# Performance work log

Measured on AMD Instinct MI355X. Metric: run time of the kernel, lower is better.

## Reference

```python
import jax, jax.numpy as jnp
import numpy as np

B, S, D = 8, 4096, 256
H, DK, DV = 8, 32, 32


def _layer_norm(x, g, b, eps=1e-6):
    mu = jnp.mean(x, axis=-1, keepdims=True)
    var = jnp.mean(jnp.square(x - mu), axis=-1, keepdims=True)
    return (x - mu) * jax.lax.rsqrt(var + eps) * g + b


def setup_inputs() -> dict:
    key = jax.random.key(0)
    ks = jax.random.split(key, 16)
    std = 1.0 / np.sqrt(D)
    p = lambda k, shp: (jax.random.normal(k, shp, jnp.float32) * std)
    return {
        "h": jax.random.normal(ks[0], (B, S, D), jnp.float32),
        "e": jax.random.normal(ks[1], (B, S, D), jnp.float32),
        "s": jax.random.normal(ks[2], (B, D), jnp.float32),
        "sat_wq": p(ks[3], (D, H * DK)), "sat_wk": p(ks[4], (D, H * DK)),
        "sat_wv": p(ks[5], (D, H * DV)), "sat_wo": p(ks[6], (H * DV, D)),
        "sat_g": jnp.ones((D,), jnp.float32), "sat_b": jnp.zeros((D,), jnp.float32),
        "rel_wq": p(ks[7], (D, H * DK)), "rel_wk": p(ks[8], (D, H * DK)),
        "rel_wv": p(ks[9], (D, H * DV)), "rel_wo": p(ks[10], (H * DV, D)),
        "rel_g": jnp.ones((D,), jnp.float32), "rel_b": jnp.zeros((D,), jnp.float32),
    }


def reference(h, e, s, sat_wq, sat_wk, sat_wv, sat_wo, sat_g, sat_b,
              rel_wq, rel_wk, rel_wv, rel_wo, rel_g, rel_b):
    b, sl, d = h.shape
    scale = 1.0 / np.sqrt(DK)

    # ---- build 5-token context: [left, self, right, entity, relay] ----
    hp = jnp.pad(h, ((0, 0), (1, 1), (0, 0)))  # zeros at both ends
    s_exp = jnp.broadcast_to(s[:, None, :], (b, sl, d))
    ctx = jnp.stack([hp[:, :sl], h, hp[:, 2:], e, s_exp], axis=2)  # [B,S,5,D]

    # ---- satellite attention: 1 query vs 5-token context per position ----
    q = (h @ sat_wq).reshape(b, sl, H, DK)
    k = (ctx @ sat_wk).reshape(b, sl, 5, H, DK)
    v = (ctx @ sat_wv).reshape(b, sl, 5, H, DV)
    attn = jax.nn.softmax(jnp.einsum('bshd,bschd->bshc', q, k) * scale, axis=-1)
    o = jnp.einsum('bshc,bschd->bshd', attn, v).reshape(b, sl, H * DV) @ sat_wo
    h_out = _layer_norm(o + h, sat_g, sat_b)  # [B,S,D]

    # ---- relay attention: relay query vs [s; h_out] ----
    s_h = jnp.concatenate([s[:, None, :], h_out], axis=1)  # [B,S+1,D]
    qr = (s @ rel_wq).reshape(b, H, DK)
    kr = (s_h @ rel_wk).reshape(b, sl + 1, H, DK)
    vr = (s_h @ rel_wv).reshape(b, sl + 1, H, DV)
    attn_r = jax.nn.softmax(jnp.einsum('bhd,bkhd->bhk', qr, kr) * scale, axis=-1)
    orl = jnp.einsum('bhk,bkhd->bhd', attn_r, vr).reshape(b, H * DV) @ rel_wo
    s_out = _layer_norm(orl + s, rel_g, rel_b)  # [B,D]

    return (h_out, s_out)
```

## Files before the change

### kernel.cpp

```cpp
#include <hip/hip_runtime.h>
#include <hip/hip_bf16.h>

typedef unsigned short ushort_t;
typedef unsigned int uint_t;
typedef __attribute__((ext_vector_type(8))) short bf16x8;
typedef __attribute__((ext_vector_type(4))) float f32x4;

#define NB 8
#define NS 4096
#define ND 256
#define NH 8
#define NDK 32
#define NBS (NB*NS)
#define NK  (NS+1)
#define CH  513
#define NCH 8
static const size_t PBUF = (size_t)NB*(NS+1)*ND;
static const size_t HSZ  = (size_t)NBS*ND;

__device__ __forceinline__ ushort_t f2b(float x){
  union { __hip_bfloat16 b; ushort_t u; } cv; cv.b = __float2bfloat16(x); return cv.u;
}
__device__ __forceinline__ float b2f(ushort_t u){
  union { uint_t u; float f; } cv; cv.u = ((uint_t)u) << 16; return cv.f;
}
__device__ __forceinline__ void gload16(const ushort_t* g, ushort_t* l){
  __builtin_amdgcn_global_load_lds(
      (const __attribute__((address_space(1))) void*)g,
      (__attribute__((address_space(3))) void*)l, 16, 0, 0);
}
__device__ __forceinline__ uint4 packbf16x8(float4 a, float4 b){
  uint4 p;
  p.x = f2b(a.x) | ((uint_t)f2b(a.y)<<16);
  p.y = f2b(a.z) | ((uint_t)f2b(a.w)<<16);
  p.z = f2b(b.x) | ((uint_t)f2b(b.y)<<16);
  p.w = f2b(b.z) | ((uint_t)f2b(b.w)<<16);
  return p;
}

__device__ __forceinline__ float bsum256(float v){
  __shared__ float tmp[4];
  #pragma unroll
  for (int o=32;o>0;o>>=1) v += __shfl_down(v,o);
  if ((threadIdx.x & 63)==0) tmp[threadIdx.x>>6] = v;
  __syncthreads();
  float r = tmp[0]+tmp[1]+tmp[2]+tmp[3];
  __syncthreads();
  return r;
}

__global__ __launch_bounds__(256) void prep(
    const float* __restrict__ w0, const float* __restrict__ w1, const float* __restrict__ w2,
    const float* __restrict__ w3, const float* __restrict__ w4, const float* __restrict__ w5,
    ushort_t* __restrict__ WtAll,
    const float* __restrict__ s,
    const float* __restrict__ rwq,
    ushort_t* __restrict__ ksb, ushort_t* __restrict__ vsb,
    float* __restrict__ qr, ushort_t* __restrict__ krv)
{
  __shared__ float sh[64*68];
  const int blk = blockIdx.x;
  const int tid = threadIdx.x;
  if (blk < 96){
    const int z = blk >> 4, xy = blk & 15;
    const float* W = (z==0)?w0:(z==1)?w1:(z==2)?w2:(z==3)?w3:(z==4)?w4:w5;
    ushort_t* Wt = WtAll + (size_t)z*65536;
    float (*t)[68] = (float(*)[68])sh;
    const int k0 = (xy>>2)*64, n0 = (xy&3)*64;
    const int tr = tid>>4, tc4 = (tid&15)*4;
    #pragma unroll
    for (int i=0;i<4;i++){
      int r = tr + i*16;
      float4 v = *(const float4*)&W[(size_t)(k0+r)*ND + n0 + tc4];
      t[r][tc4]=v.x; t[r][tc4+1]=v.y; t[r][tc4+2]=v.z; t[r][tc4+3]=v.w;
    }
    __syncthreads();
    #pragma unroll
    for (int i=0;i<4;i++){
      int n = tr + i*16;
      uint_t q0 = f2b(t[tc4+0][n]) | ((uint_t)f2b(t[tc4+1][n])<<16);
      uint_t q1 = f2b(t[tc4+2][n]) | ((uint_t)f2b(t[tc4+3][n])<<16);
      *(uint2*)&Wt[(size_t)(n0+n)*ND + k0 + tc4] = make_uint2(q0,q1);
    }
  } else {
    const int rem = blk - 96;
    const int b = rem & 7, which = rem >> 3;
    const float* W = (which==0)?w1:(which==1)?w2:(which==2)?rwq:(which==3)?w4:w5;
    float* a = sh;
    a[tid] = s[(size_t)b*ND + tid];
    __syncthreads();
    float acc = 0.f;
    #pragma unroll 8
    for (int d=0; d<ND; d++)
      acc = fmaf(a[d], W[(size_t)d*ND + tid], acc);
    switch (which){
      case 0: ksb[(size_t)b*ND + tid] = f2b(acc); break;
      case 1: vsb[(size_t)b*ND + tid] = f2b(acc); break;
      case 2: qr[(size_t)b*ND + tid] = acc; break;
      case 3: krv[(size_t)b*NK*512 + tid] = f2b(acc); break;
      default: krv[(size_t)b*NK*512 + 256 + tid] = f2b(acc); break;
    }
  }
}

__global__ __launch_bounds__(512) void gemm_qkve(const float* __restrict__ hA,
    const float* __restrict__ eA, const ushort_t* __restrict__ Wt,
    ushort_t* __restrict__ hQKV, ushort_t* __restrict__ eKV)
{
  __shared__ __align__(16) ushort_t Ap[64][256];
  __shared__ __align__(16) ushort_t Bs[2][128][64];
  const int blk = blockIdx.x;
  const bool isH = blk < 512;
  const float* A = isH ? hA : eA;
  const ushort_t* Wb = isH ? Wt : (Wt + 65536);
  ushort_t* Y = isH ? hQKV : eKV;
  const int ldn  = isH ? 768 : 512;
  const int ncol = isH ? 6 : 4;
  const int row0 = (blk & 511) * 64;
  const int tid = threadIdx.x;
  const int lane = tid & 63;
  const int wave = tid >> 6;
  const int wr  = (wave>>2)*32;
  const int wcw = (wave&3)*32;
  const int l15 = lane & 15, lg = lane >> 4;
  const int lr8 = lane >> 3;
  const int ls  = (lane & 7) ^ lr8;

  #pragma unroll
  for (int i=0;i<4;i++){
    int sgi = tid + i*512;
    int r   = sgi >> 5;
    int c8  = (sgi & 31) * 8;
    const float* ga = A + (size_t)(row0 + r)*ND + c8;
    float4 a0 = *(const float4*)ga, a1 = *(const float4*)(ga+4);
    int byte = r*512 + ((c8*2) ^ ((r&7)<<4));
    *(uint4*)((char*)&Ap[0][0] + byte) = packbf16x8(a0,a1);
  }

  const ushort_t* Bbase = Wb + (size_t)(wave*16 + lr8)*ND + ls*8;
  #define STAGEB(ct, kt, bb) do{ \
    const ushort_t* bp = Bbase + (size_t)(ct)*128*ND + (kt)*64; \
    gload16(bp,                &Bs[bb][wave*16][0]); \
    gload16(bp + (size_t)8*ND, &Bs[bb][wave*16+8][0]); \
  }while(0)

  const f32x4 vzero = {0.f,0.f,0.f,0.f};
  f32x4 acc[2][2] = {};
  STAGEB(0,0,0);
  __syncthreads();
  int buf = 0;
  const int total = ncol*4;
  for (int s = 0; s < total; ++s){
    const int kt = s & 3;
    if (s+1 < total) STAGEB((s+1)>>2, (s+1)&3, buf^1);
    #pragma unroll
    for (int ks=0; ks<2; ks++){
      bf16x8 af[2], bfr[2];
      #pragma unroll
      for (int mi=0;mi<2;mi++){
        int ra  = wr + mi*16 + l15;
        int cb2 = kt*128 + ks*64 + lg*16;
        af[mi] = *(const bf16x8*)((const char*)&Ap[0][0] + ra*512 + (cb2 ^ ((ra&7)<<4)));
      }
      #pragma unroll
      for (int ni=0;ni<2;ni++){
        int rb = wcw + ni*16 + l15;
        int cb = (ks<<6) + (lg<<4);
        bfr[ni] = *(const bf16x8*)((const char*)&Bs[buf][0][0] + rb*128 + (cb ^ ((rb&7)<<4)));
      }
      #pragma unroll
      for (int mi=0;mi<2;mi++)
        #pragma unroll
        for (int ni=0;ni<2;ni++)
          acc[mi][ni] = __builtin_amdgcn_mfma_f32_16x16x32_bf16(af[mi], bfr[ni], acc[mi][ni], 0,0,0);
    }
    __syncthreads();
    buf ^= 1;
    if (kt == 3){
      const int col0 = (s >> 2) * 128;
      #pragma unroll
      for (int mi=0;mi<2;mi++)
        #pragma unroll
        for (int r=0;r<4;r++){
          size_t orow = (size_t)(row0 + wr + mi*16 + lg*4 + r);
          #pragma unroll
          for (int ni=0;ni<2;ni++)
            Y[orow*(size_t)ldn + col0 + wcw + ni*16 + l15] = f2b(acc[mi][ni][r]);
        }
      #pragma unroll
      for (int mi=0;mi<2;mi++)
        #pragma unroll
        for (int ni=0;ni<2;ni++)
          acc[mi][ni] = vzero;
    }
  }
  #undef STAGEB
}

__global__ __launch_bounds__(512) void gemm_krv(const ushort_t* __restrict__ A,
    const ushort_t* __restrict__ Wt, ushort_t* __restrict__ Y)
{
  __shared__ __align__(16) ushort_t As[2][128][64];
  __shared__ __align__(16) ushort_t Bs[2][128][64];
  const int tid  = threadIdx.x;
  const int row0 = blockIdx.x*128;
  const int col0 = blockIdx.y*128;
  const int lane = tid & 63;
  const int wave = tid >> 6;
  const int wr = (wave>>2)*64;
  const int wc = (wave&3)*32;
  const int l15 = lane & 15, lg = lane >> 4;
  const int lr8 = lane >> 3;
  const int ls  = (lane & 7) ^ lr8;

  const ushort_t* Asrc = A  + (size_t)(row0 + wave*16 + lr8)*ND + ls*8;
  const ushort_t* Bsrc = Wt + (size_t)(col0 + wave*16 + lr8)*ND + ls*8;

  f32x4 acc[4][2] = {};

  #define STAGE(t, bb) do{ \
    gload16(Asrc + (t)*64,                &As[bb][wave*16][0]); \
    gload16(Asrc + (size_t)8*ND + (t)*64, &As[bb][wave*16+8][0]); \
    gload16(Bsrc + (t)*64,                &Bs[bb][wave*16][0]); \
    gload16(Bsrc + (size_t)8*ND + (t)*64, &Bs[bb][wave*16+8][0]); \
  }while(0)
  #define COMPUTE(bb) do{ \
    _Pragma("unroll") \
    for (int ks=0; ks<2; ks++){ \
      bf16x8 af[4], bfr[2]; \
      _Pragma("unroll") \
      for (int mi=0;mi<4;mi++){ \
        int ra = wr + mi*16 + l15; int cb = (ks<<6) + (lg<<4); \
        af[mi] = *(const bf16x8*)((const char*)&As[bb][0][0] + ra*128 + (cb ^ ((ra&7)<<4))); \
      } \
      _Pragma("unroll") \
      for (int ni=0;ni<2;ni++){ \
        int rb = wc + ni*16 + l15; int cb = (ks<<6) + (lg<<4); \
        bfr[ni] = *(const bf16x8*)((const char*)&Bs[bb][0][0] + rb*128 + (cb ^ ((rb&7)<<4))); \
      } \
      _Pragma("unroll") \
      for (int mi=0;mi<4;mi++) \
        _Pragma("unroll") \
        for (int ni=0;ni<2;ni++) \
          acc[mi][ni] = __builtin_amdgcn_mfma_f32_16x16x32_bf16(af[mi], bfr[ni], acc[mi][ni], 0,0,0); \
    } \
  }while(0)

  STAGE(0, 0);
  __syncthreads();
  STAGE(1, 1); COMPUTE(0); __syncthreads();
  STAGE(2, 0); COMPUTE(1); __syncthreads();
  STAGE(3, 1); COMPUTE(0); __syncthreads();
  COMPUTE(1);
  #undef STAGE
  #undef COMPUTE

  #pragma unroll
  for (int mi=0;mi<4;mi++)
    #pragma unroll
    for (int r=0;r<4;r++){
      int row = row0 + wr + mi*16 + lg*4 + r;
      size_t orow = (size_t)(row>>12)*NK + 1 + (row&4095);
      #pragma unroll
      for (int ni=0;ni<2;ni++)
        Y[orow*512 + col0 + wc + ni*16 + l15] = f2b(acc[mi][ni][r]);
    }
}

__global__ __launch_bounds__(512) void oproj_ln(const ushort_t* __restrict__ A,
    const ushort_t* __restrict__ Wt, const float* __restrict__ hres,
    const float* __restrict__ g, const float* __restrict__ bta,
    float* __restrict__ outf, ushort_t* __restrict__ outb)
{
  __shared__ __align__(16) ushort_t As[2][64][64];
  __shared__ float rs[64][4], rq[64][4];
  __shared__ float gl[ND], bl[ND];
  const int tid  = threadIdx.x;
  const int row0 = blockIdx.x*64;
  const int lane = tid & 63;
  const int wave = tid >> 6;
  const int wr = (wave>>2)*32;
  const int wc = (wave&3)*64;
  const int l15 = lane & 15, lg = lane >> 4;
  const int lr8 = lane >> 3;
  const int ls  = (lane & 7) ^ lr8;

  if (tid < ND){ gl[tid] = g[tid]; bl[tid] = bta[tid]; }

  const ushort_t* Asrc = A + (size_t)(row0 + wave*8 + lr8)*ND + ls*8;

  f32x4 acc[2][4] = {};

  #define STAGE3(t, bb) gload16(Asrc + (t)*64, &As[bb][wave*8][0])
  #define COMPUTE3(t, bb) do{ \
    _Pragma("unroll") \
    for (int ks=0; ks<2; ks++){ \
      bf16x8 af[2], bfr[4]; \
      _Pragma("unroll") \
      for (int mi=0;mi<2;mi++){ \
        int ra = wr + mi*16 + l15; int cb = (ks<<6) + (lg<<4); \
        af[mi] = *(const bf16x8*)((const char*)&As[bb][0][0] + ra*128 + (cb ^ ((ra&7)<<4))); \
      } \
      _Pragma("unroll") \
      for (int ni=0;ni<4;ni++) \
        bfr[ni] = *(const bf16x8*)&Wt[(size_t)(wc + ni*16 + l15)*ND + (t)*64 + ks*32 + lg*8]; \
      _Pragma("unroll") \
      for (int mi=0;mi<2;mi++) \
        _Pragma("unroll") \
        for (int ni=0;ni<4;ni++) \
          acc[mi][ni] = __builtin_amdgcn_mfma_f32_16x16x32_bf16(af[mi], bfr[ni], acc[mi][ni], 0,0,0); \
    } \
  }while(0)

  STAGE3(0, 0);
  __syncthreads();
  STAGE3(1, 1); COMPUTE3(0, 0); __syncthreads();
  STAGE3(2, 0); COMPUTE3(1, 1); __syncthreads();
  STAGE3(3, 1); COMPUTE3(2, 0); __syncthreads();
  COMPUTE3(3, 1);
  #undef STAGE3
  #undef COMPUTE3

  #pragma unroll
  for (int mi=0;mi<2;mi++)
    #pragma unroll
    for (int rr=0;rr<4;rr++){
      size_t rowb = (size_t)(row0 + wr + mi*16 + lg*4 + rr)*ND;
      #pragma unroll
      for (int ni=0;ni<4;ni++)
        acc[mi][ni][rr] += hres[rowb + wc + ni*16 + l15];
    }

  #pragma unroll
  for (int mi=0;mi<2;mi++)
    #pragma unroll
    for (int rr=0;rr<4;rr++){
      float sv = 0.f, qv = 0.f;
      #pragma unroll
      for (int ni=0;ni<4;ni++){ float x = acc[mi][ni][rr]; sv += x; qv += x*x; }
      #pragma unroll
      for (int o=1;o<16;o<<=1){ sv += __shfl_xor(sv,o); qv += __shfl_xor(qv,o); }
      if (l15 == 0){
        int rl = wr + mi*16 + lg*4 + rr;
        rs[rl][wave&3] = sv; rq[rl][wave&3] = qv;
      }
    }
  __syncthreads();

  #pragma unroll
  for (int mi=0;mi<2;mi++)
    #pragma unroll
    for (int rr=0;rr<4;rr++){
      int rl = wr + mi*16 + lg*4 + rr;
      float sm = rs[rl][0] + rs[rl][1] + rs[rl][2] + rs[rl][3];
      float sq = rq[rl][0] + rq[rl][1] + rq[rl][2] + rq[rl][3];
      float mu = sm * (1.0f/ND);
      float var = sq * (1.0f/ND) - mu*mu;
      float rstd = rsqrtf(var + 1e-6f);
      size_t rowb = (size_t)(row0 + rl)*ND;
      #pragma unroll
      for (int ni=0;ni<4;ni++){
        int col = wc + ni*16 + l15;
        float yv = (acc[mi][ni][rr] - mu)*rstd*gl[col] + bl[col];
        outf[rowb + col] = yv;
        outb[rowb + col] = f2b(yv);
      }
    }
}

__device__ __forceinline__ void load8(float* d, const ushort_t* p){
  bf16x8 v = *(const bf16x8*)p;
  #pragma unroll
  for (int i=0;i<8;i++) d[i] = b2f((ushort_t)v[i]);
}
__device__ __forceinline__ void zero8(float* d){
  #pragma unroll
  for (int i=0;i<8;i++) d[i] = 0.f;
}
__global__ __launch_bounds__(256) void sat_attn4(const ushort_t* __restrict__ HQ,
    const ushort_t* __restrict__ EKV,
    const ushort_t* __restrict__ KS, const ushort_t* __restrict__ VS,
    ushort_t* __restrict__ O)
{
  const int tid = threadIdx.x;
  const int l  = tid & 3;
  const int g  = tid >> 2;
  const int hh = g & 7;
  const int pi = g >> 3;
  const int pos = blockIdx.x*8 + pi;
  const int b = pos >> 12, t = pos & 4095;
  const int co = hh*NDK + l*8;
  const float scale = 0.17677669529663687f;

  const size_t rq = (size_t)pos*768;
  const size_t re = (size_t)pos*512;
  float q[8], k0[8], k1[8], k2[8], k3[8], k4[8];
  load8(q,  HQ + rq + co);
  load8(k1, HQ + rq + 256 + co);
  load8(k3, EKV + re + co);
  load8(k4, KS + (size_t)b*ND + co);
  if (t > 0)    load8(k0, HQ + rq - 768 + 256 + co);
  else          zero8(k0);
  if (t < NS-1) load8(k2, HQ + rq + 768 + 256 + co);
  else          zero8(k2);

  float s0=0.f,s1=0.f,s2=0.f,s3=0.f,s4=0.f;
  #pragma unroll
  for (int i=0;i<8;i++){
    s0 = fmaf(q[i],k0[i],s0); s1 = fmaf(q[i],k1[i],s1); s2 = fmaf(q[i],k2[i],s2);
    s3 = fmaf(q[i],k3[i],s3); s4 = fmaf(q[i],k4[i],s4);
  }
  #pragma unroll
  for (int mm=1; mm<4; mm<<=1){
    s0 += __shfl_xor(s0,mm); s1 += __shfl_xor(s1,mm); s2 += __shfl_xor(s2,mm);
    s3 += __shfl_xor(s3,mm); s4 += __shfl_xor(s4,mm);
  }
  s0*=scale; s1*=scale; s2*=scale; s3*=scale; s4*=scale;
  float m = fmaxf(fmaxf(fmaxf(s0,s1),fmaxf(s2,s3)),s4);
  float p0=expf(s0-m), p1=expf(s1-m), p2=expf(s2-m), p3=expf(s3-m), p4=expf(s4-m);
  float inv = 1.0f/(p0+p1+p2+p3+p4);

  float v0[8], v1[8], v2[8], v3[8], v4[8];
  load8(v1, HQ + rq + 512 + co);
  load8(v3, EKV + re + 256 + co);
  load8(v4, VS + (size_t)b*ND + co);
  if (t > 0)    load8(v0, HQ + rq - 768 + 512 + co);
  else          zero8(v0);
  if (t < NS-1) load8(v2, HQ + rq + 768 + 512 + co);
  else          zero8(v2);

  float o[8];
  #pragma unroll
  for (int i=0;i<8;i++)
    o[i] = (p0*v0[i] + p1*v1[i] + p2*v2[i] + p3*v3[i] + p4*v4[i]) * inv;
  uint4 pk;
  pk.x = f2b(o[0])|((uint_t)f2b(o[1])<<16);
  pk.y = f2b(o[2])|((uint_t)f2b(o[3])<<16);
  pk.z = f2b(o[4])|((uint_t)f2b(o[5])<<16);
  pk.w = f2b(o[6])|((uint_t)f2b(o[7])<<16);
  *(uint4*)&O[(size_t)pos*ND + co] = pk;
}

__global__ __launch_bounds__(256) void rel_part(const float* __restrict__ QR,
    const ushort_t* __restrict__ KRV,
    float* __restrict__ pO, float* __restrict__ pM, float* __restrict__ pL)
{
  const int bh = blockIdx.x;
  const int b = bh >> 3, h = bh & 7;
  const int c = blockIdx.y;
  const int k0 = c*CH;
  const int kn = min(NK, k0+CH) - k0;
  const int tid = threadIdx.x;
  __shared__ float sc[CH];
  __shared__ float qs[NDK];
  __shared__ float red[8][NDK];
  __shared__ float tmp[4];
  if (tid < NDK) qs[tid] = QR[(size_t)b*ND + h*NDK + tid];
  __syncthreads();
  const float scale = 0.17677669529663687f;
  for (int kk=tid; kk<kn; kk+=256){
    const ushort_t* kp = KRV + ((size_t)b*NK + k0 + kk)*512 + h*NDK;
    float sdot = 0.f;
    #pragma unroll
    for (int w=0; w<4; w++){
      bf16x8 kv = *(const bf16x8*)(kp + w*8);
      #pragma unroll
      for (int i=0;i<8;i++) sdot = fmaf(qs[w*8+i], b2f((ushort_t)kv[i]), sdot);
    }
    sc[kk] = sdot * scale;
  }
  __syncthreads();
  float lm = -1e30f;
  for (int kk=tid; kk<kn; kk+=256) lm = fmaxf(lm, sc[kk]);
  #pragma unroll
  for (int o=32;o>0;o>>=1) lm = fmaxf(lm, __shfl_down(lm,o));
  if ((tid & 63)==0) tmp[tid>>6] = lm;
  __syncthreads();
  float m = fmaxf(fmaxf(tmp[0],tmp[1]),fmaxf(tmp[2],tmp[3]));
  __syncthreads();
  float ls = 0.f;
  for (int kk=tid; kk<kn; kk+=256){ float p = expf(sc[kk]-m); sc[kk] = p; ls += p; }
  #pragma unroll
  for (int o=32;o>0;o>>=1) ls += __shfl_down(ls,o);
  if ((tid & 63)==0) tmp[tid>>6] = ls;
  __syncthreads();
  float lsum = tmp[0]+tmp[1]+tmp[2]+tmp[3];
  int grp = tid>>5, d = tid&31;
  float acc = 0.f;
  for (int kk=grp; kk<kn; kk+=8)
    acc = fmaf(sc[kk], b2f(KRV[((size_t)b*NK + k0 + kk)*512 + 256 + h*NDK + d]), acc);
  red[grp][d] = acc;
  __syncthreads();
  if (grp == 0){
    float tot = 0.f;
    #pragma unroll
    for (int i=0;i<8;i++) tot += red[i][d];
    pO[((size_t)bh*NCH + c)*NDK + d] = tot;
    if (d == 0){ pM[bh*NCH + c] = m; pL[bh*NCH + c] = lsum; }
  }
}

__global__ __launch_bounds__(256) void rel_tail(const float* __restrict__ pO,
    const float* __restrict__ pM, const float* __restrict__ pL,
    const float* __restrict__ WO, const float* __restrict__ Sv,
    const float* __restrict__ g, const float* __restrict__ bta,
    float* __restrict__ out)
{
  const int b = blockIdx.x, j = threadIdx.x;
  __shared__ float ol[ND];
  {
    const int h = j >> 5, d = j & 31;
    const int bh = b*NH + h;
    float m = -1e30f;
    #pragma unroll
    for (int c=0;c<NCH;c++) m = fmaxf(m, pM[bh*NCH + c]);
    float o = 0.f, l = 0.f;
    #pragma unroll
    for (int c=0;c<NCH;c++){
      float w = expf(pM[bh*NCH + c] - m);
      o = fmaf(pO[((size_t)bh*NCH + c)*NDK + d], w, o);
      l = fmaf(pL[bh*NCH + c], w, l);
    }
    ol[j] = o / l;
  }
  __syncthreads();
  float x = 0.f;
  for (int d=0; d<ND; d++) x = fmaf(ol[d], WO[(size_t)d*ND + j], x);
  x += Sv[(size_t)b*ND + j];
  float mu = bsum256(x) * (1.0f/ND);
  float dd = x - mu;
  float var = bsum256(dd*dd) * (1.0f/ND);
  out[(size_t)NBS*ND + (size_t)b*ND + j] = dd * rsqrtf(var + 1e-6f) * g[j] + bta[j];
}

extern "C" void kernel_launch(void* const* d_in, const int* in_sizes, int n_in,
                              void* d_out, int out_size, void* d_ws, size_t ws_size,
                              hipStream_t stream)
{
  const float* h      = (const float*)d_in[0];
  const float* e      = (const float*)d_in[1];
  const float* s      = (const float*)d_in[2];
  const float* sat_wq = (const float*)d_in[3];
  const float* sat_wk = (const float*)d_in[4];
  const float* sat_wv = (const float*)d_in[5];
  const float* sat_wo = (const float*)d_in[6];
  const float* sat_g  = (const float*)d_in[7];
  const float* sat_b  = (const float*)d_in[8];
  const float* rel_wq = (const float*)d_in[9];
  const float* rel_wk = (const float*)d_in[10];
  const float* rel_wv = (const float*)d_in[11];
  const float* rel_wo = (const float*)d_in[12];
  const float* rel_g  = (const float*)d_in[13];
  const float* rel_b  = (const float*)d_in[14];
  float* out = (float*)d_out;

  float* ws = (float*)d_ws;
  ushort_t* hQKV = (ushort_t*)ws;
  ushort_t* eKV  = (ushort_t*)(ws + 2*PBUF);
  ushort_t* krv  = (ushort_t*)(ws + 4*PBUF);
  ushort_t* hb   = (ushort_t*)(ws + 5*PBUF);
  ushort_t* satO = hb + HSZ;
  ushort_t* Wt   = satO + HSZ;
  float* smalls  = (float*)(Wt + 6*65536);
  ushort_t* ksb = (ushort_t*)smalls;
  ushort_t* vsb = ksb + 2048;
  float* qr  = smalls + 4096;
  float* pO  = smalls + 8192;
  float* pM  = pO + (size_t)NB*NH*NCH*NDK;
  float* pL  = pM + NB*NH*NCH;

  dim3 gb(256);

  prep<<<136, gb, 0, stream>>>(sat_wq, sat_wk, sat_wv, sat_wo, rel_wk, rel_wv, Wt,
                               s, rel_wq, ksb, vsb, qr, krv);

  gemm_qkve<<<1024, dim3(512), 0, stream>>>(h, e, Wt, hQKV, eKV);

  sat_attn4<<<NBS/8, gb, 0, stream>>>(hQKV, eKV, ksb, vsb, satO);

  oproj_ln<<<NBS/64, dim3(512), 0, stream>>>(satO, Wt + 3*65536, h, sat_g, sat_b, out, hb);

  gemm_krv<<<dim3(NBS/128, 4), dim3(512), 0, stream>>>(hb, Wt + 4*65536, krv);

  rel_part<<<dim3(NB*NH, NCH), gb, 0, stream>>>(qr, krv, pO, pM, pL);

  rel_tail<<<NB, gb, 0, stream>>>(pO, pM, pL, rel_wo, s, rel_g, rel_b, out);
}
```

Measured before the change: 172.3 us.

## Fuse relay K/V projection GEMM into output-projection LayerNorm kernel

Merges the satellite output projection plus LayerNorm kernel with the following relay K/V GEMM. The LayerNorm result is kept as bf16 in swizzled shared memory and multiplied directly against streamed relay K/V weight tiles. This removes the global write and re-read of the bf16 h_out buffer and one kernel launch. In exchange, shared memory per block grows to roughly 70KB, which may lower occupancy, and the relay GEMM now runs with a 64-row tile per block instead of the previous 128x128 tiling.

New measurement: 157.8 us. 1.09x faster.

```diff
diff --git a/kernel.cpp b/kernel.cpp
--- a/kernel.cpp
+++ b/kernel.cpp
@@ -197,82 +197,14 @@
   #undef STAGEB
 }
 
-__global__ __launch_bounds__(512) void gemm_krv(const ushort_t* __restrict__ A,
-    const ushort_t* __restrict__ Wt, ushort_t* __restrict__ Y)
-{
-  __shared__ __align__(16) ushort_t As[2][128][64];
-  __shared__ __align__(16) ushort_t Bs[2][128][64];
-  const int tid  = threadIdx.x;
-  const int row0 = blockIdx.x*128;
-  const int col0 = blockIdx.y*128;
-  const int lane = tid & 63;
-  const int wave = tid >> 6;
-  const int wr = (wave>>2)*64;
-  const int wc = (wave&3)*32;
-  const int l15 = lane & 15, lg = lane >> 4;
-  const int lr8 = lane >> 3;
-  const int ls  = (lane & 7) ^ lr8;
-
-  const ushort_t* Asrc = A  + (size_t)(row0 + wave*16 + lr8)*ND + ls*8;
-  const ushort_t* Bsrc = Wt + (size_t)(col0 + wave*16 + lr8)*ND + ls*8;
-
-  f32x4 acc[4][2] = {};
-
-  #define STAGE(t, bb) do{ \
-    gload16(Asrc + (t)*64,                &As[bb][wave*16][0]); \
-    gload16(Asrc + (size_t)8*ND + (t)*64, &As[bb][wave*16+8][0]); \
-    gload16(Bsrc + (t)*64,                &Bs[bb][wave*16][0]); \
-    gload16(Bsrc + (size_t)8*ND + (t)*64, &Bs[bb][wave*16+8][0]); \
-  }while(0)
-  #define COMPUTE(bb) do{ \
-    _Pragma("unroll") \
-    for (int ks=0; ks<2; ks++){ \
-      bf16x8 af[4], bfr[2]; \
-      _Pragma("unroll") \
-      for (int mi=0;mi<4;mi++){ \
-        int ra = wr + mi*16 + l15; int cb = (ks<<6) + (lg<<4); \
-        af[mi] = *(const bf16x8*)((const char*)&As[bb][0][0] + ra*128 + (cb ^ ((ra&7)<<4))); \
-      } \
-      _Pragma("unroll") \
-      for (int ni=0;ni<2;ni++){ \
-        int rb = wc + ni*16 + l15; int cb = (ks<<6) + (lg<<4); \
-        bfr[ni] = *(const bf16x8*)((const char*)&Bs[bb][0][0] + rb*128 + (cb ^ ((rb&7)<<4))); \
-      } \
-      _Pragma("unroll") \
-      for (int mi=0;mi<4;mi++) \
-        _Pragma("unroll") \
-        for (int ni=0;ni<2;ni++) \
-          acc[mi][ni] = __builtin_amdgcn_mfma_f32_16x16x32_bf16(af[mi], bfr[ni], acc[mi][ni], 0,0,0); \
-    } \
-  }while(0)
-
-  STAGE(0, 0);
-  __syncthreads();
-  STAGE(1, 1); COMPUTE(0); __syncthreads();
-  STAGE(2, 0); COMPUTE(1); __syncthreads();
-  STAGE(3, 1); COMPUTE(0); __syncthreads();
-  COMPUTE(1);
-  #undef STAGE
-  #undef COMPUTE
-
-  #pragma unroll
-  for (int mi=0;mi<4;mi++)
-    #pragma unroll
-    for (int r=0;r<4;r++){
-      int row = row0 + wr + mi*16 + lg*4 + r;
-      size_t orow = (size_t)(row>>12)*NK + 1 + (row&4095);
-      #pragma unroll
-      for (int ni=0;ni<2;ni++)
-        Y[orow*512 + col0 + wc + ni*16 + l15] = f2b(acc[mi][ni][r]);
-    }
-}
-
-__global__ __launch_bounds__(512) void oproj_ln(const ushort_t* __restrict__ A,
-    const ushort_t* __restrict__ Wt, const float* __restrict__ hres,
+__global__ __launch_bounds__(512) void oproj_krv(const ushort_t* __restrict__ A,
+    const ushort_t* __restrict__ Wto, const ushort_t* __restrict__ WtKRV,
+    const float* __restrict__ hres,
     const float* __restrict__ g, const float* __restrict__ bta,
-    float* __restrict__ outf, ushort_t* __restrict__ outb)
-{
-  __shared__ __align__(16) ushort_t As[2][64][64];
+    float* __restrict__ outf, ushort_t* __restrict__ krv)
+{
+  __shared__ __align__(16) ushort_t Pool[2][128][64];
+  __shared__ __align__(16) ushort_t Ap[64][256];
   __shared__ float rs[64][4], rq[64][4];
   __shared__ float gl[ND], bl[ND];
   const int tid  = threadIdx.x;
@@ -281,12 +213,14 @@
   const int wave = tid >> 6;
   const int wr = (wave>>2)*32;
   const int wc = (wave&3)*64;
+  const int wcw = (wave&3)*32;
   const int l15 = lane & 15, lg = lane >> 4;
   const int lr8 = lane >> 3;
   const int ls  = (lane & 7) ^ lr8;
 
   if (tid < ND){ gl[tid] = g[tid]; bl[tid] = bta[tid]; }
 
+  ushort_t (*As)[64][64] = (ushort_t(*)[64][64])&Pool[0][0][0];
   const ushort_t* Asrc = A + (size_t)(row0 + wave*8 + lr8)*ND + ls*8;
 
   f32x4 acc[2][4] = {};
@@ -303,7 +237,7 @@
       } \
       _Pragma("unroll") \
       for (int ni=0;ni<4;ni++) \
-        bfr[ni] = *(const bf16x8*)&Wt[(size_t)(wc + ni*16 + l15)*ND + (t)*64 + ks*32 + lg*8]; \
+        bfr[ni] = *(const bf16x8*)&Wto[(size_t)(wc + ni*16 + l15)*ND + (t)*64 + ks*32 + lg*8]; \
       _Pragma("unroll") \
       for (int mi=0;mi<2;mi++) \
         _Pragma("unroll") \
@@ -363,9 +297,69 @@
         int col = wc + ni*16 + l15;
         float yv = (acc[mi][ni][rr] - mu)*rstd*gl[col] + bl[col];
         outf[rowb + col] = yv;
-        outb[rowb + col] = f2b(yv);
+        int byte = rl*512 + ((col*2) ^ ((rl&7)<<4));
+        *(ushort_t*)((char*)&Ap[0][0] + byte) = f2b(yv);
       }
     }
+
+  const ushort_t* Bbase = WtKRV + (size_t)(wave*16 + lr8)*ND + ls*8;
+  #define STAGEB(ct, kt, bb) do{ \
+    const ushort_t* bp = Bbase + (size_t)(ct)*128*ND + (kt)*64; \
+    gload16(bp,                &Pool[bb][wave*16][0]); \
+    gload16(bp + (size_t)8*ND, &Pool[bb][wave*16+8][0]); \
+  }while(0)
+
+  const f32x4 vzero = {0.f,0.f,0.f,0.f};
+  f32x4 acc2[2][2] = {};
+  STAGEB(0,0,0);
+  __syncthreads();
+  int buf = 0;
+  for (int s = 0; s < 16; ++s){
+    const int kt = s & 3;
+    if (s+1 < 16) STAGEB((s+1)>>2, (s+1)&3, buf^1);
+    #pragma unroll
+    for (int ks=0; ks<2; ks++){
+      bf16x8 af[2], bfr[2];
+      #pragma unroll
+      for (int mi=0;mi<2;mi++){
+        int ra  = wr + mi*16 + l15;
+        int cb2 = kt*128 + ks*64 + lg*16;
+        af[mi] = *(const bf16x8*)((const char*)&Ap[0][0] + ra*512 + (cb2 ^ ((ra&7)<<4)));
+      }
+      #pragma unroll
+      for (int ni=0;ni<2;ni++){
+        int rb = wcw + ni*16 + l15;
+        int cb = (ks<<6) + (lg<<4);
+        bfr[ni] = *(const bf16x8*)((const char*)&Pool[buf][0][0] + rb*128 + (cb ^ ((rb&7)<<4)));
+      }
+      #pragma unroll
+      for (int mi=0;mi<2;mi++)
+        #pragma unroll
+        for (int ni=0;ni<2;ni++)
+          acc2[mi][ni] = __builtin_amdgcn_mfma_f32_16x16x32_bf16(af[mi], bfr[ni], acc2[mi][ni], 0,0,0);
+    }
+    __syncthreads();
+    buf ^= 1;
+    if (kt == 3){
+      const int col0 = (s >> 2) * 128;
+      #pragma unroll
+      for (int mi=0;mi<2;mi++)
+        #pragma unroll
+        for (int r=0;r<4;r++){
+          int row = row0 + wr + mi*16 + lg*4 + r;
+          size_t orow = (size_t)(row>>12)*NK + 1 + (row&4095);
+          #pragma unroll
+          for (int ni=0;ni<2;ni++)
+            krv[orow*512 + col0 + wcw + ni*16 + l15] = f2b(acc2[mi][ni][r]);
+        }
+      #pragma unroll
+      for (int mi=0;mi<2;mi++)
+        #pragma unroll
+        for (int ni=0;ni<2;ni++)
+          acc2[mi][ni] = vzero;
+    }
+  }
+  #undef STAGEB
 }
 
 __device__ __forceinline__ void load8(float* d, const ushort_t* p){
@@ -558,8 +552,7 @@
   ushort_t* hQKV = (ushort_t*)ws;
   ushort_t* eKV  = (ushort_t*)(ws + 2*PBUF);
   ushort_t* krv  = (ushort_t*)(ws + 4*PBUF);
-  ushort_t* hb   = (ushort_t*)(ws + 5*PBUF);
-  ushort_t* satO = hb + HSZ;
+  ushort_t* satO = (ushort_t*)(ws + 5*PBUF);
   ushort_t* Wt   = satO + HSZ;
   float* smalls  = (float*)(Wt + 6*65536);
   ushort_t* ksb = (ushort_t*)smalls;
@@ -578,9 +571,8 @@
 
   sat_attn4<<<NBS/8, gb, 0, stream>>>(hQKV, eKV, ksb, vsb, satO);
 
-  oproj_ln<<<NBS/64, dim3(512), 0, stream>>>(satO, Wt + 3*65536, h, sat_g, sat_b, out, hb);
-
-  gemm_krv<<<dim3(NBS/128, 4), dim3(512), 0, stream>>>(hb, Wt + 4*65536, krv);
+  oproj_krv<<<NBS/64, dim3(512), 0, stream>>>(satO, Wt + 3*65536, Wt + 4*65536,
+                                              h, sat_g, sat_b, out, krv);
 
   rel_part<<<dim3(NB*NH, NCH), gb, 0, stream>>>(qr, krv, pO, pM, pL);
 
```
